# Performance work log

Measured on AMD Instinct MI355X. Metric: run time of the kernel, lower is better.

The kernel has to match this reference:

```python
import jax, jax.numpy as jnp
import numpy as np

N_NODES = 100000
N_EDGES = 1600000
IN_DIM = 128
HEADS = 4
HID = 32            # per-head channels; HEADS*HID == 128 == IN_DIM
HC = HEADS * HID
NUM_CLASSES = 349
NUM_LAYERS = 2
BN_EPS = 1e-5
NEG_SLOPE = 0.2     # PyG GATConv default leaky_relu slope


def _gat_conv(x, src, dst, Wsrc, Wdst, a_src, a_dst, bias):
    """PyG GATConv (concat=True). x:[N,F] -> [N,H*C]."""
    N = x.shape[0]
    xs = (x @ Wsrc).reshape(N, HEADS, HID)   # source-side projection
    xd = (x @ Wdst).reshape(N, HEADS, HID)   # dest-side projection
    s_src = jnp.einsum('nhc,hc->nh', xs, a_src)   # [N,H]
    s_dst = jnp.einsum('nhc,hc->nh', xd, a_dst)   # [N,H]
    e = jax.nn.leaky_relu(s_src[src] + s_dst[dst], NEG_SLOPE)   # [E,H]
    # numerically-stable edge softmax grouped by destination node
    m = jax.ops.segment_max(e, dst, num_segments=N)             # [N,H]
    m = jnp.where(jnp.isfinite(m), m, 0.0)                      # isolated nodes
    p = jnp.exp(e - m[dst])                                     # [E,H]
    denom = jax.ops.segment_sum(p, dst, num_segments=N)         # [N,H]
    alpha = p / (denom[dst] + 1e-16)                            # [E,H]
    msg = xs[src] * alpha[:, :, None]                           # [E,H,C]
    out = jax.ops.segment_sum(msg, dst, num_segments=N)         # [N,H,C]
    return out.reshape(N, HC) + bias


def _batch_norm(x, gamma, beta):
    mu = x.mean(0)
    var = x.var(0)
    return gamma * (x - mu) * jax.lax.rsqrt(var + BN_EPS) + beta


def setup_inputs() -> dict:
    key = jax.random.key(0)
    ks = jax.random.split(key, 8)
    sc = 1.0 / np.sqrt(IN_DIM)
    inp = {
        'x': jax.random.normal(ks[0], (N_NODES, IN_DIM), jnp.float32),
        'edge_index': jax.random.randint(ks[1], (2, N_EDGES), 0, N_NODES, jnp.int32),
        'W_src': jax.random.normal(ks[2], (NUM_LAYERS, IN_DIM, HC), jnp.float32) * sc,
        'W_dst': jax.random.normal(ks[3], (NUM_LAYERS, IN_DIM, HC), jnp.float32) * sc,
        'att_src': jax.random.normal(ks[4], (NUM_LAYERS, HEADS, HID), jnp.float32) * sc,
        'att_dst': jax.random.normal(ks[5], (NUM_LAYERS, HEADS, HID), jnp.float32) * sc,
        'conv_bias': jnp.zeros((NUM_LAYERS, HC), jnp.float32),
        'lin_W': jax.random.normal(ks[6], (NUM_LAYERS, IN_DIM, HC), jnp.float32) * sc,
        'lin_b': jnp.zeros((NUM_LAYERS, HC), jnp.float32),
        'bn_gamma': jnp.ones((NUM_LAYERS, HC), jnp.float32),
        'bn_beta': jnp.zeros((NUM_LAYERS, HC), jnp.float32),
        'fc_W': jax.random.normal(ks[7], (IN_DIM, NUM_CLASSES), jnp.float32) * sc,
        'fc_b': jnp.zeros((NUM_CLASSES,), jnp.float32),
    }
    return inp


def reference(x, edge_index, W_src, W_dst, att_src, att_dst, conv_bias,
              lin_W, lin_b, bn_gamma, bn_beta, fc_W, fc_b):
    src, dst = edge_index[0], edge_index[1]
    for i in range(NUM_LAYERS):
        h = _gat_conv(x, src, dst, W_src[i], W_dst[i], att_src[i], att_dst[i],
                      conv_bias[i])
        h = h + x @ lin_W[i] + lin_b[i]          # skip projection
        h = _batch_norm(h, bn_gamma[i], bn_beta[i])
        x = jax.nn.relu(h)                        # dropout p=0.2 omitted (eval)
    return x @ fc_W + fc_b
```

## Files before the change

### kernel.cpp

```cpp
#include <hip/hip_runtime.h>
#include <hip/hip_bf16.h>
#include <stdint.h>

#define N_NODES 100000
#define N_EDGES 1600000
#define IN_DIM 128
#define HEADS 4
#define HID 32
#define HC 128
#define NUM_CLASSES 349
#define NUM_LAYERS 2
#define BN_EPS 1e-5f
#define NEG_SLOPE 0.2f
#define NCAT 264
#define MP 100032

#define NPARAM 144861

#define NBKT 782
#define ECHUNK 8192
#define NCHUNK ((N_EDGES + ECHUNK - 1) / ECHUNK)
#define NTOT (NBKT * NCHUNK)
#define SCAN_CHUNK 1024
#define SCAN2_BLOCKS ((NTOT + SCAN_CHUNK - 1) / SCAN_CHUNK)

using bf16 = __hip_bfloat16;
typedef __attribute__((ext_vector_type(8))) short short8;
typedef __attribute__((ext_vector_type(4))) float floatx4;

__device__ __forceinline__ float b2f(bf16 v) { return __bfloat162float(v); }

__global__ void detect_dtype(const uint32_t* __restrict__ xw, int* __restrict__ flag) {
    int lane = threadIdx.x;
    int insane = 0;
    for (int i = lane; i < 256; i += 64) {
        uint32_t lo = xw[i] & 0xffffu;
        uint32_t e = (lo >> 7) & 0xffu;
        if (lo != 0u && (e < 100u || e > 150u)) insane++;
    }
    for (int off = 32; off > 0; off >>= 1) insane += __shfl_down(insane, off, 64);
    if (lane == 0) *flag = (insane > 64) ? 1 : 0;
}

__global__ void cvt_xb(const void* __restrict__ in, bf16* __restrict__ out,
                       int n, int npad, const int* __restrict__ flag) {
    bool isf32 = (*flag != 0);
    int i = blockIdx.x * blockDim.x + threadIdx.x;
    int stride = gridDim.x * blockDim.x;
    for (; i < npad; i += stride) {
        bf16 v = __float2bfloat16(0.f);
        if (i < n) v = isf32 ? __float2bfloat16(((const float*)in)[i]) : ((const bf16*)in)[i];
        out[i] = v;
    }
}

__global__ void cvt_params(const void* p0, const void* p1, const void* p2, const void* p3,
                           const void* p4, const void* p5, const void* p6, const void* p7,
                           const void* p8, const void* p9, const void* p10,
                           float* __restrict__ out, const int* __restrict__ flag) {
    int i = blockIdx.x * blockDim.x + threadIdx.x;
    if (i >= NPARAM) return;
    bool isf32 = (*flag != 0);
    const void* p; int off;
    if      (i < 32768)  { p = p0;  off = i; }
    else if (i < 65536)  { p = p1;  off = i - 32768; }
    else if (i < 65792)  { p = p2;  off = i - 65536; }
    else if (i < 66048)  { p = p3;  off = i - 65792; }
    else if (i < 66304)  { p = p4;  off = i - 66048; }
    else if (i < 99072)  { p = p5;  off = i - 66304; }
    else if (i < 99328)  { p = p6;  off = i - 99072; }
    else if (i < 99584)  { p = p7;  off = i - 99328; }
    else if (i < 99840)  { p = p8;  off = i - 99584; }
    else if (i < 144512) { p = p9;  off = i - 99840; }
    else                 { p = p10; off = i - 144512; }
    out[i] = isf32 ? ((const float*)p)[off] : b2f(((const bf16*)p)[off]);
}

__global__ void build_bcat(const float* __restrict__ Wsrc, const float* __restrict__ Wdst,
                           const float* __restrict__ asrc, const float* __restrict__ adst,
                           const float* __restrict__ linW, float* __restrict__ B) {
    int idx = blockIdx.x * blockDim.x + threadIdx.x;
    if (idx >= IN_DIM * NCAT) return;
    int k = idx / NCAT, j = idx - k * NCAT;
    float v;
    if (j < 128) {
        v = Wsrc[k * HC + j];
    } else if (j < 132) {
        int h = j - 128; float s = 0.f;
        for (int c = 0; c < HID; c++) s += Wsrc[k * HC + h * HID + c] * asrc[h * HID + c];
        v = s;
    } else if (j < 136) {
        int h = j - 132; float s = 0.f;
        for (int c = 0; c < HID; c++) s += Wdst[k * HC + h * HID + c] * adst[h * HID + c];
        v = s;
    } else {
        v = linW[k * HC + (j - 136)];
    }
    B[idx] = v;
}

__global__ void pack_b(const float* __restrict__ src, int ld, int nvalid,
                       bf16* __restrict__ Bp, int total) {
    int idx = blockIdx.x * blockDim.x + threadIdx.x;
    if (idx >= total) return;
    int j = idx & 7, lane = (idx >> 3) & 63, kt = (idx >> 9) & 3, nt = idx >> 11;
    int n = nt * 16 + (lane & 15);
    int k = kt * 32 + ((lane >> 4) << 3) + j;
    float v = (n < nvalid) ? src[k * ld + n] : 0.f;
    Bp[idx] = __float2bfloat16(v);
}

template <int BNMODE>
__global__ __launch_bounds__(256) void gemm_mfma_proj(
    const bf16* __restrict__ A, const bf16* __restrict__ Bp,
    bf16* __restrict__ xs, bf16* __restrict__ scA, bf16* __restrict__ xlin,
    const float* __restrict__ gamma, const float* __restrict__ beta,
    const float* __restrict__ bnsum, const float* __restrict__ bnsq) {
    __shared__ bf16 As[64 * 128];
    int tid = threadIdx.x;
    size_t rowbase = (size_t)blockIdx.x * 64;
    const int4* ga = (const int4*)(A + rowbase * 128);
    int4* la = (int4*)As;
    const float invN = 1.f / (float)N_NODES;
#pragma unroll
    for (int s = 0; s < 4; s++) {
        int4 raw = ga[s * 256 + tid];
        if (BNMODE) {
            bf16* hv = (bf16*)&raw;
            int cbase = ((s * 256 + tid) & 15) * 8;
            int4 outv; bf16* ov = (bf16*)&outv;
#pragma unroll
            for (int j = 0; j < 8; j++) {
                int c = cbase + j;
                float mu = bnsum[c] * invN;
                float var = bnsq[c] * invN - mu * mu;
                float v = gamma[c] * (b2f(hv[j]) - mu) * rsqrtf(var + BN_EPS) + beta[c];
                ov[j] = __float2bfloat16(v > 0.f ? v : 0.f);
            }
            la[s * 256 + tid] = outv;
        } else {
            la[s * 256 + tid] = raw;
        }
    }
    __syncthreads();
    int wave = tid >> 6, lane = tid & 63;
    int arow = wave * 16 + (lane & 15);
    int acol = (lane >> 4) * 8;
    short8 afrag[4];
#pragma unroll
    for (int kt = 0; kt < 4; kt++)
        afrag[kt] = *(const short8*)&As[arow * 128 + kt * 32 + acol];
    const short8* bbase = (const short8*)Bp + lane;
    int colb = lane & 15;
    int row0 = wave * 16 + (lane >> 4) * 4;
#pragma unroll
    for (int nt = 0; nt < 17; nt++) {
        floatx4 acc = {0.f, 0.f, 0.f, 0.f};
#pragma unroll
        for (int kt = 0; kt < 4; kt++)
            acc = __builtin_amdgcn_mfma_f32_16x16x32_bf16(afrag[kt], bbase[(nt * 4 + kt) * 64], acc, 0, 0, 0);
        int col = nt * 16 + colb;
#pragma unroll
        for (int r = 0; r < 4; r++) {
            size_t row = rowbase + row0 + r;
            bf16 v = __float2bfloat16(acc[r]);
            if (col < 128)       xs[row * HC + col] = v;
            else if (col < 136)  scA[row * 8 + (col - 128)] = v;
            else { int q = col - 136; if (q < 128) xlin[row * HC + q] = v; }
        }
    }
}

__global__ __launch_bounds__(256) void gemm_mfma_out(
    const bf16* __restrict__ A, const bf16* __restrict__ Bp,
    const float* __restrict__ bias,
    const float* __restrict__ gamma, const float* __restrict__ beta,
    const float* __restrict__ bnsum, const float* __restrict__ bnsq,
    void* __restrict__ C, const int* __restrict__ flag) {
    __shared__ bf16 As[64 * 128];
    int tid = threadIdx.x;
    size_t rowbase = (size_t)blockIdx.x * 64;
    const int4* ga = (const int4*)(A + rowbase * 128);
    int4* la = (int4*)As;
    const float invN = 1.f / (float)N_NODES;
#pragma unroll
    for (int s = 0; s < 4; s++) {
        int4 raw = ga[s * 256 + tid];
        bf16* hv = (bf16*)&raw;
        int cbase = ((s * 256 + tid) & 15) * 8;
        int4 outv; bf16* ov = (bf16*)&outv;
#pragma unroll
        for (int j = 0; j < 8; j++) {
            int c = cbase + j;
            float mu = bnsum[c] * invN;
            float var = bnsq[c] * invN - mu * mu;
            float v = gamma[c] * (b2f(hv[j]) - mu) * rsqrtf(var + BN_EPS) + beta[c];
            ov[j] = __float2bfloat16(v > 0.f ? v : 0.f);
        }
        la[s * 256 + tid] = outv;
    }
    __syncthreads();
    int wave = tid >> 6, lane = tid & 63;
    int arow = wave * 16 + (lane & 15);
    int acol = (lane >> 4) * 8;
    short8 afrag[4];
#pragma unroll
    for (int kt = 0; kt < 4; kt++)
        afrag[kt] = *(const short8*)&As[arow * 128 + kt * 32 + acol];
    const short8* bbase = (const short8*)Bp + lane;
    int colb = lane & 15;
    int row0 = wave * 16 + (lane >> 4) * 4;
    bool isf32 = (*flag != 0);
    for (int nt = 0; nt < 22; nt++) {
        floatx4 acc = {0.f, 0.f, 0.f, 0.f};
#pragma unroll
        for (int kt = 0; kt < 4; kt++)
            acc = __builtin_amdgcn_mfma_f32_16x16x32_bf16(afrag[kt], bbase[(nt * 4 + kt) * 64], acc, 0, 0, 0);
        int col = nt * 16 + colb;
        if (col >= NUM_CLASSES) continue;
        float bv = bias[col];
#pragma unroll
        for (int r = 0; r < 4; r++) {
            size_t row = rowbase + row0 + r;
            if (row < N_NODES) {
                float v = acc[r] + bv;
                if (isf32) ((float*)C)[row * NUM_CLASSES + col] = v;
                else       ((bf16*)C)[row * NUM_CLASSES + col] = __float2bfloat16(v);
            }
        }
    }
}

__global__ __launch_bounds__(256) void bucket_hist(const int* __restrict__ dst,
                                                   int* __restrict__ cnt) {
    __shared__ int h[NBKT];
    int t = threadIdx.x;
    for (int i = t; i < NBKT; i += 256) h[i] = 0;
    __syncthreads();
    int base = blockIdx.x * ECHUNK;
    int end = base + ECHUNK; if (end > N_EDGES) end = N_EDGES;
    for (int i = base + t; i < end; i += 256)
        atomicAdd(&h[dst[i] >> 7], 1);
    __syncthreads();
    for (int i = t; i < NBKT; i += 256)
        cnt[i * NCHUNK + blockIdx.x] = h[i];
}

__global__ void scan_partial(const int* __restrict__ counts, int* __restrict__ bsum, int n) {
    __shared__ int red[256];
    int t = threadIdx.x;
    int base = blockIdx.x * SCAN_CHUNK + t * 4;
    int s = 0;
#pragma unroll
    for (int j = 0; j < 4; j++) {
        int idx = base + j;
        if (idx < n) s += counts[idx];
    }
    red[t] = s;
    __syncthreads();
    for (int off = 128; off > 0; off >>= 1) {
        if (t < off) red[t] += red[t + off];
        __syncthreads();
    }
    if (t == 0) bsum[blockIdx.x] = red[0];
}

__global__ void scan_bsums(int* __restrict__ bsum, int nblocks) {
    if (threadIdx.x != 0 || blockIdx.x != 0) return;
    int run = 0;
    for (int i = 0; i < nblocks; i++) {
        int v = bsum[i];
        bsum[i] = run;
        run += v;
    }
}

__global__ void scan_final(int* __restrict__ counts, const int* __restrict__ bsum, int n) {
    __shared__ int ts[256];
    int t = threadIdx.x;
    int base = blockIdx.x * SCAN_CHUNK + t * 4;
    int c[4];
    int mysum = 0;
#pragma unroll
    for (int j = 0; j < 4; j++) {
        int idx = base + j;
        c[j] = (idx < n) ? counts[idx] : 0;
        mysum += c[j];
    }
    ts[t] = mysum;
    __syncthreads();
    for (int off = 1; off < 256; off <<= 1) {
        int v = (t >= off) ? ts[t - off] : 0;
        __syncthreads();
        ts[t] += v;
        __syncthreads();
    }
    int run = bsum[blockIdx.x] + ts[t] - mysum;
#pragma unroll
    for (int j = 0; j < 4; j++) {
        int idx = base + j;
        if (idx < n) {
            counts[idx] = run;
            run += c[j];
        }
    }
}

__global__ __launch_bounds__(256) void bucket_scatter(const int* __restrict__ src,
                                                      const int* __restrict__ dst,
                                                      const int* __restrict__ cntscan,
                                                      uint32_t* __restrict__ sorted) {
    __shared__ int cur[NBKT];
    int t = threadIdx.x;
    for (int i = t; i < NBKT; i += 256)
        cur[i] = cntscan[i * NCHUNK + blockIdx.x];
    __syncthreads();
    int base = blockIdx.x * ECHUNK;
    int end = base + ECHUNK; if (end > N_EDGES) end = N_EDGES;
    for (int i = base + t; i < end; i += 256) {
        int d = dst[i];
        int b = d >> 7;
        int pos = atomicAdd(&cur[b], 1);
        sorted[pos] = ((uint32_t)(d & 127) << 17) | (uint32_t)src[i];
    }
}

__global__ __launch_bounds__(256) void bucket_csr(const uint32_t* __restrict__ sorted,
                                                  const int* __restrict__ cntscan,
                                                  int* __restrict__ srcs,
                                                  int* __restrict__ offsets) {
    __shared__ int cnt128[128];
    __shared__ int sc[128];
    __shared__ int cur[128];
    int b = blockIdx.x, t = threadIdx.x;
    int ebeg = cntscan[b * NCHUNK];
    int eend = (b == NBKT - 1) ? N_EDGES : cntscan[(b + 1) * NCHUNK];
    if (t < 128) cnt128[t] = 0;
    __syncthreads();
    uint32_t buf[10];
    int k = 0;
    for (int e = ebeg + t; e < eend; e += 256) {
        uint32_t u = sorted[e];
        if (k < 10) buf[k] = u;
        k++;
        atomicAdd(&cnt128[u >> 17], 1);
    }
    __syncthreads();
    if (t < 128) sc[t] = cnt128[t];
    __syncthreads();
    for (int off = 1; off < 128; off <<= 1) {
        int v = 0;
        if (t < 128 && t >= off) v = sc[t - off];
        __syncthreads();
        if (t < 128) sc[t] += v;
        __syncthreads();
    }
    if (t < 128) {
        int node = b * 128 + t;
        if (node < N_NODES) offsets[node] = ebeg + sc[t];
        cur[t] = ebeg + sc[t] - cnt128[t];
    }
    __syncthreads();
    int k2 = 0;
    for (int e = ebeg + t; e < eend; e += 256) {
        uint32_t u = (k2 < 10) ? buf[k2] : sorted[e];
        k2++;
        int ld = (int)(u >> 17);
        int pos = atomicAdd(&cur[ld], 1);
        srcs[pos] = (int)(u & 0x1FFFFu);
    }
}

__device__ __forceinline__ void edge_acc(int s, int h, int c0, float s_dst,
                                         const bf16* __restrict__ xs,
                                         const bf16* __restrict__ scA,
                                         float& den, float& n0, float& n1) {
    float sc = b2f(scA[(size_t)s * 8 + h]) + s_dst;
    sc = sc > 0.f ? sc : NEG_SLOPE * sc;
    float e = __expf(sc);
    __hip_bfloat162 xv = *reinterpret_cast<const __hip_bfloat162*>(&xs[(size_t)s * HC + c0]);
    den += e;
    n0 += b2f(xv.x) * e;
    n1 += b2f(xv.y) * e;
}

__global__ __launch_bounds__(256) void gat_gather(
    const int* __restrict__ srcs, const int* __restrict__ offsets,
    const bf16* __restrict__ xs, const bf16* __restrict__ scA,
    const bf16* __restrict__ xlin,
    const float* __restrict__ cbias, const float* __restrict__ lbias,
    bf16* __restrict__ hout) {
    int n = blockIdx.x * 4 + (threadIdx.x >> 6);
    int lane = threadIdx.x & 63;
    int c0 = lane * 2;
    int h = c0 >> 5;
    int beg = (n == 0) ? 0 : offsets[n - 1];
    int end = offsets[n];
    float s_dst = b2f(scA[(size_t)n * 8 + 4 + h]);
    float den = 0.f, n0 = 0.f, n1 = 0.f;
    int i = beg;
    for (; i + 3 < end; i += 4) {
        int s0 = srcs[i], s1 = srcs[i + 1], s2 = srcs[i + 2], s3 = srcs[i + 3];
        edge_acc(s0, h, c0, s_dst, xs, scA, den, n0, n1);
        edge_acc(s1, h, c0, s_dst, xs, scA, den, n0, n1);
        edge_acc(s2, h, c0, s_dst, xs, scA, den, n0, n1);
        edge_acc(s3, h, c0, s_dst, xs, scA, den, n0, n1);
    }
    for (; i < end; i++)
        edge_acc(srcs[i], h, c0, s_dst, xs, scA, den, n0, n1);
    float r = 1.f / (den + 1e-16f);
    __hip_bfloat162 xl = *reinterpret_cast<const __hip_bfloat162*>(&xlin[(size_t)n * HC + c0]);
    float v0 = n0 * r + b2f(xl.x) + cbias[c0] + lbias[c0];
    float v1 = n1 * r + b2f(xl.y) + cbias[c0 + 1] + lbias[c0 + 1];
    __hip_bfloat162 hv;
    hv.x = __float2bfloat16(v0);
    hv.y = __float2bfloat16(v1);
    *reinterpret_cast<__hip_bfloat162*>(&hout[(size_t)n * HC + c0]) = hv;
}

__global__ void bn_stats(const bf16* __restrict__ h, float* __restrict__ bnsum,
                         float* __restrict__ bnsq) {
    int c = threadIdx.x & 127;
    int half = threadIdx.x >> 7;
    int r0 = blockIdx.x * 500;
    int rend = r0 + 500; if (rend > N_NODES) rend = N_NODES;
    float s1 = 0.f, s2 = 0.f;
    for (int r = r0 + half; r < rend; r += 2) {
        float v = b2f(h[(size_t)r * HC + c]);
        s1 += v; s2 += v * v;
    }
    atomicAdd(&bnsum[c], s1);
    atomicAdd(&bnsq[c], s2);
}

extern "C" void kernel_launch(void* const* d_in, const int* in_sizes, int n_in,
                              void* d_out, int out_size, void* d_ws, size_t ws_size,
                              hipStream_t stream) {
    const void* x_in = d_in[0];
    const int*  edge = (const int*)d_in[1];
    const int* esrc = edge;
    const int* edst = edge + N_EDGES;

    bf16* xbh  = (bf16*)d_ws;
    bf16* xs   = xbh + (size_t)MP * HC;
    bf16* scA  = xs + (size_t)MP * HC;
    bf16* xlin = scA + (size_t)MP * 8;
    float* Bcat = (float*)(xlin + (size_t)MP * HC);
    bf16* Bp   = (bf16*)(Bcat + IN_DIM * NCAT);
    bf16* fcWp = Bp + 17 * 2048;
    float* bnstat = (float*)(fcWp + 22 * 2048);
    int*   flag  = (int*)(bnstat + 512);
    int*   bsum  = flag + 4;
    float* parms = (float*)(bsum + SCAN2_BLOCKS + 2);
    float* Wsrc_f  = parms;
    float* Wdst_f  = parms + 32768;
    float* asrc_f  = parms + 65536;
    float* adst_f  = parms + 65792;
    float* cbias_f = parms + 66048;
    float* linW_f  = parms + 66304;
    float* linb_f  = parms + 99072;
    float* gamma_f = parms + 99328;
    float* beta_f  = parms + 99584;
    float* fcW_f   = parms + 99840;
    float* fcb_f   = parms + 144512;

    int* srcs    = (int*)d_out;
    int* offsets = srcs + N_EDGES;
    uint32_t* sorted = (uint32_t*)(offsets + N_NODES);
    int* cnt = (int*)(sorted + N_EDGES);

    detect_dtype<<<1, 64, 0, stream>>>((const uint32_t*)x_in, flag);

    cvt_xb<<<1024, 256, 0, stream>>>(x_in, xbh, N_NODES * HC, MP * HC, flag);
    cvt_params<<<(NPARAM + 255) / 256, 256, 0, stream>>>(
        d_in[2], d_in[3], d_in[4], d_in[5], d_in[6], d_in[7], d_in[8],
        d_in[9], d_in[10], d_in[11], d_in[12], parms, flag);

    bucket_hist<<<NCHUNK, 256, 0, stream>>>(edst, cnt);
    scan_partial<<<SCAN2_BLOCKS, 256, 0, stream>>>(cnt, bsum, NTOT);
    scan_bsums<<<1, 64, 0, stream>>>(bsum, SCAN2_BLOCKS);
    scan_final<<<SCAN2_BLOCKS, 256, 0, stream>>>(cnt, bsum, NTOT);
    bucket_scatter<<<NCHUNK, 256, 0, stream>>>(esrc, edst, cnt, sorted);
    bucket_csr<<<NBKT, 256, 0, stream>>>(sorted, cnt, srcs, offsets);

    pack_b<<<(22 * 2048 + 255) / 256, 256, 0, stream>>>(fcW_f, NUM_CLASSES, NUM_CLASSES,
                                                        fcWp, 22 * 2048);
    hipMemsetAsync(bnstat, 0, 512 * sizeof(float), stream);

    for (int layer = 0; layer < NUM_LAYERS; layer++) {
        const int woff = layer * IN_DIM * HC;
        const int aoff = layer * HEADS * HID;
        const int boff = layer * HC;
        float* bns = bnstat + layer * 256;
        float* bnq = bns + 128;

        build_bcat<<<(IN_DIM * NCAT + 255) / 256, 256, 0, stream>>>(
            Wsrc_f + woff, Wdst_f + woff, asrc_f + aoff, adst_f + aoff,
            linW_f + woff, Bcat);
        pack_b<<<(17 * 2048 + 255) / 256, 256, 0, stream>>>(Bcat, NCAT, NCAT,
                                                            Bp, 17 * 2048);

        if (layer == 0) {
            gemm_mfma_proj<0><<<MP / 64, 256, 0, stream>>>(
                xbh, Bp, xs, scA, xlin, nullptr, nullptr, nullptr, nullptr);
        } else {
            float* pbns = bnstat + (layer - 1) * 256;
            gemm_mfma_proj<1><<<MP / 64, 256, 0, stream>>>(
                xbh, Bp, xs, scA, xlin,
                gamma_f + (layer - 1) * HC, beta_f + (layer - 1) * HC,
                pbns, pbns + 128);
        }

        gat_gather<<<N_NODES / 4, 256, 0, stream>>>(
            srcs, offsets, xs, scA, xlin, cbias_f + boff, linb_f + boff, xbh);

        bn_stats<<<200, 256, 0, stream>>>(xbh, bns, bnq);
    }

    gemm_mfma_out<<<MP / 64, 256, 0, stream>>>(
        xbh, fcWp, fcb_f, gamma_f + HC, beta_f + HC,
        bnstat + 256, bnstat + 256 + 128, d_out, flag);
}
```

Baseline: 758.2 us.

## Fuse input conversion into projection GEMM, merge weight packing, drop serial scan

Removes the separate x-to-bf16 conversion kernel: the layer-0 projection GEMM now reads the raw input (fp32 or bf16) and converts it while staging into shared memory. build_bcat and pack_b are merged so the concatenated weights go straight into the packed MFMA layout. The single-thread block-sum scan is dropped, and each scan_final block instead reduces the prefix of bsum itself. The gather loop also gains an 8-way unrolled edge loop. Together these cut kernel launches and one full pass over x, at the cost of redundant prefix reductions across scan blocks and higher register use in the gather.

Result: faster. 703.1 us (-7.3%).

```diff
diff --git a/kernel.cpp b/kernel.cpp
--- a/kernel.cpp
+++ b/kernel.cpp
@@ -40,18 +40,6 @@
     }
     for (int off = 32; off > 0; off >>= 1) insane += __shfl_down(insane, off, 64);
     if (lane == 0) *flag = (insane > 64) ? 1 : 0;
-}
-
-__global__ void cvt_xb(const void* __restrict__ in, bf16* __restrict__ out,
-                       int n, int npad, const int* __restrict__ flag) {
-    bool isf32 = (*flag != 0);
-    int i = blockIdx.x * blockDim.x + threadIdx.x;
-    int stride = gridDim.x * blockDim.x;
-    for (; i < npad; i += stride) {
-        bf16 v = __float2bfloat16(0.f);
-        if (i < n) v = isf32 ? __float2bfloat16(((const float*)in)[i]) : ((const bf16*)in)[i];
-        out[i] = v;
-    }
 }
 
 __global__ void cvt_params(const void* p0, const void* p1, const void* p2, const void* p3,
@@ -76,27 +64,27 @@
     out[i] = isf32 ? ((const float*)p)[off] : b2f(((const bf16*)p)[off]);
 }
 
-__global__ void build_bcat(const float* __restrict__ Wsrc, const float* __restrict__ Wdst,
-                           const float* __restrict__ asrc, const float* __restrict__ adst,
-                           const float* __restrict__ linW, float* __restrict__ B) {
+__global__ void pack_bcat(const float* __restrict__ Wsrc, const float* __restrict__ Wdst,
+                          const float* __restrict__ asrc, const float* __restrict__ adst,
+                          const float* __restrict__ linW, bf16* __restrict__ Bp) {
     int idx = blockIdx.x * blockDim.x + threadIdx.x;
-    if (idx >= IN_DIM * NCAT) return;
-    int k = idx / NCAT, j = idx - k * NCAT;
-    float v;
-    if (j < 128) {
-        v = Wsrc[k * HC + j];
-    } else if (j < 132) {
-        int h = j - 128; float s = 0.f;
-        for (int c = 0; c < HID; c++) s += Wsrc[k * HC + h * HID + c] * asrc[h * HID + c];
-        v = s;
-    } else if (j < 136) {
-        int h = j - 132; float s = 0.f;
-        for (int c = 0; c < HID; c++) s += Wdst[k * HC + h * HID + c] * adst[h * HID + c];
-        v = s;
-    } else {
-        v = linW[k * HC + (j - 136)];
-    }
-    B[idx] = v;
+    if (idx >= 17 * 2048) return;
+    int j = idx & 7, lane = (idx >> 3) & 63, kt = (idx >> 9) & 3, nt = idx >> 11;
+    int n = nt * 16 + (lane & 15);
+    int k = kt * 32 + ((lane >> 4) << 3) + j;
+    float v = 0.f;
+    if (n < 128) {
+        v = Wsrc[k * HC + n];
+    } else if (n < 132) {
+        int h = n - 128;
+        for (int c = 0; c < HID; c++) v += Wsrc[k * HC + h * HID + c] * asrc[h * HID + c];
+    } else if (n < 136) {
+        int h = n - 132;
+        for (int c = 0; c < HID; c++) v += Wdst[k * HC + h * HID + c] * adst[h * HID + c];
+    } else if (n < 264) {
+        v = linW[k * HC + (n - 136)];
+    }
+    Bp[idx] = __float2bfloat16(v);
 }
 
 __global__ void pack_b(const float* __restrict__ src, int ld, int nvalid,
@@ -110,22 +98,48 @@
     Bp[idx] = __float2bfloat16(v);
 }
 
-template <int BNMODE>
+template <int MODE>
 __global__ __launch_bounds__(256) void gemm_mfma_proj(
-    const bf16* __restrict__ A, const bf16* __restrict__ Bp,
+    const void* __restrict__ Araw, const int* __restrict__ flag,
+    const bf16* __restrict__ Bp,
     bf16* __restrict__ xs, bf16* __restrict__ scA, bf16* __restrict__ xlin,
     const float* __restrict__ gamma, const float* __restrict__ beta,
     const float* __restrict__ bnsum, const float* __restrict__ bnsq) {
     __shared__ bf16 As[64 * 128];
     int tid = threadIdx.x;
     size_t rowbase = (size_t)blockIdx.x * 64;
-    const int4* ga = (const int4*)(A + rowbase * 128);
     int4* la = (int4*)As;
     const float invN = 1.f / (float)N_NODES;
-#pragma unroll
-    for (int s = 0; s < 4; s++) {
-        int4 raw = ga[s * 256 + tid];
-        if (BNMODE) {
+    if (MODE == 0) {
+        bool isf32 = (*flag != 0);
+#pragma unroll
+        for (int s = 0; s < 4; s++) {
+            int idx = s * 256 + tid;
+            size_t grow = rowbase + (idx >> 4);
+            int cg = idx & 15;
+            int4 outv = {0, 0, 0, 0};
+            if (grow < N_NODES) {
+                if (isf32) {
+                    const float* xr = (const float*)Araw + grow * 128 + cg * 8;
+                    float4 f0 = ((const float4*)xr)[0];
+                    float4 f1 = ((const float4*)xr)[1];
+                    bf16* ov = (bf16*)&outv;
+                    ov[0] = __float2bfloat16(f0.x); ov[1] = __float2bfloat16(f0.y);
+                    ov[2] = __float2bfloat16(f0.z); ov[3] = __float2bfloat16(f0.w);
+                    ov[4] = __float2bfloat16(f1.x); ov[5] = __float2bfloat16(f1.y);
+                    ov[6] = __float2bfloat16(f1.z); ov[7] = __float2bfloat16(f1.w);
+                } else {
+                    outv = ((const int4*)Araw)[grow * 16 + cg];
+                }
+            }
+            la[idx] = outv;
+        }
+    } else {
+        const bf16* A = (const bf16*)Araw;
+        const int4* ga = (const int4*)(A + rowbase * 128);
+#pragma unroll
+        for (int s = 0; s < 4; s++) {
+            int4 raw = ga[s * 256 + tid];
             bf16* hv = (bf16*)&raw;
             int cbase = ((s * 256 + tid) & 15) * 8;
             int4 outv; bf16* ov = (bf16*)&outv;
@@ -138,8 +152,6 @@
                 ov[j] = __float2bfloat16(v > 0.f ? v : 0.f);
             }
             la[s * 256 + tid] = outv;
-        } else {
-            la[s * 256 + tid] = raw;
         }
     }
     __syncthreads();
@@ -265,19 +277,12 @@
     if (t == 0) bsum[blockIdx.x] = red[0];
 }
 
-__global__ void scan_bsums(int* __restrict__ bsum, int nblocks) {
-    if (threadIdx.x != 0 || blockIdx.x != 0) return;
-    int run = 0;
-    for (int i = 0; i < nblocks; i++) {
-        int v = bsum[i];
-        bsum[i] = run;
-        run += v;
-    }
-}
-
 __global__ void scan_final(int* __restrict__ counts, const int* __restrict__ bsum, int n) {
     __shared__ int ts[256];
+    __shared__ int pre[256];
     int t = threadIdx.x;
+    int pv = (t < (int)blockIdx.x) ? bsum[t] : 0;
+    pre[t] = pv;
     int base = blockIdx.x * SCAN_CHUNK + t * 4;
     int c[4];
     int mysum = 0;
@@ -289,13 +294,17 @@
     }
     ts[t] = mysum;
     __syncthreads();
+    for (int off = 128; off > 0; off >>= 1) {
+        if (t < off) pre[t] += pre[t + off];
+        __syncthreads();
+    }
     for (int off = 1; off < 256; off <<= 1) {
         int v = (t >= off) ? ts[t - off] : 0;
         __syncthreads();
         ts[t] += v;
         __syncthreads();
     }
-    int run = bsum[blockIdx.x] + ts[t] - mysum;
+    int run = pre[0] + ts[t] - mysum;
 #pragma unroll
     for (int j = 0; j < 4; j++) {
         int idx = base + j;
@@ -399,6 +408,18 @@
     float s_dst = b2f(scA[(size_t)n * 8 + 4 + h]);
     float den = 0.f, n0 = 0.f, n1 = 0.f;
     int i = beg;
+    for (; i + 7 < end; i += 8) {
+        int s0 = srcs[i],     s1 = srcs[i + 1], s2 = srcs[i + 2], s3 = srcs[i + 3];
+        int s4 = srcs[i + 4], s5 = srcs[i + 5], s6 = srcs[i + 6], s7 = srcs[i + 7];
+        edge_acc(s0, h, c0, s_dst, xs, scA, den, n0, n1);
+        edge_acc(s1, h, c0, s_dst, xs, scA, den, n0, n1);
+        edge_acc(s2, h, c0, s_dst, xs, scA, den, n0, n1);
+        edge_acc(s3, h, c0, s_dst, xs, scA, den, n0, n1);
+        edge_acc(s4, h, c0, s_dst, xs, scA, den, n0, n1);
+        edge_acc(s5, h, c0, s_dst, xs, scA, den, n0, n1);
+        edge_acc(s6, h, c0, s_dst, xs, scA, den, n0, n1);
+        edge_acc(s7, h, c0, s_dst, xs, scA, den, n0, n1);
+    }
     for (; i + 3 < end; i += 4) {
         int s0 = srcs[i], s1 = srcs[i + 1], s2 = srcs[i + 2], s3 = srcs[i + 3];
         edge_acc(s0, h, c0, s_dst, xs, scA, den, n0, n1);
@@ -445,8 +466,7 @@
     bf16* xs   = xbh + (size_t)MP * HC;
     bf16* scA  = xs + (size_t)MP * HC;
     bf16* xlin = scA + (size_t)MP * 8;
-    float* Bcat = (float*)(xlin + (size_t)MP * HC);
-    bf16* Bp   = (bf16*)(Bcat + IN_DIM * NCAT);
+    bf16* Bp   = xlin + (size_t)MP * HC;
     bf16* fcWp = Bp + 17 * 2048;
     float* bnstat = (float*)(fcWp + 22 * 2048);
     int*   flag  = (int*)(bnstat + 512);
@@ -471,14 +491,12 @@
 
     detect_dtype<<<1, 64, 0, stream>>>((const uint32_t*)x_in, flag);
 
-    cvt_xb<<<1024, 256, 0, stream>>>(x_in, xbh, N_NODES * HC, MP * HC, flag);
     cvt_params<<<(NPARAM + 255) / 256, 256, 0, stream>>>(
         d_in[2], d_in[3], d_in[4], d_in[5], d_in[6], d_in[7], d_in[8],
         d_in[9], d_in[10], d_in[11], d_in[12], parms, flag);
 
     bucket_hist<<<NCHUNK, 256, 0, stream>>>(edst, cnt);
     scan_partial<<<SCAN2_BLOCKS, 256, 0, stream>>>(cnt, bsum, NTOT);
-    scan_bsums<<<1, 64, 0, stream>>>(bsum, SCAN2_BLOCKS);
     scan_final<<<SCAN2_BLOCKS, 256, 0, stream>>>(cnt, bsum, NTOT);
     bucket_scatter<<<NCHUNK, 256, 0, stream>>>(esrc, edst, cnt, sorted);
     bucket_csr<<<NBKT, 256, 0, stream>>>(sorted, cnt, srcs, offsets);
@@ -494,19 +512,17 @@
         float* bns = bnstat + layer * 256;
         float* bnq = bns + 128;
 
-        build_bcat<<<(IN_DIM * NCAT + 255) / 256, 256, 0, stream>>>(
+        pack_bcat<<<(17 * 2048 + 255) / 256, 256, 0, stream>>>(
             Wsrc_f + woff, Wdst_f + woff, asrc_f + aoff, adst_f + aoff,
-            linW_f + woff, Bcat);
-        pack_b<<<(17 * 2048 + 255) / 256, 256, 0, stream>>>(Bcat, NCAT, NCAT,
-                                                            Bp, 17 * 2048);
+            linW_f + woff, Bp);
 
         if (layer == 0) {
             gemm_mfma_proj<0><<<MP / 64, 256, 0, stream>>>(
-                xbh, Bp, xs, scA, xlin, nullptr, nullptr, nullptr, nullptr);
+                x_in, flag, Bp, xs, scA, xlin, nullptr, nullptr, nullptr, nullptr);
         } else {
             float* pbns = bnstat + (layer - 1) * 256;
             gemm_mfma_proj<1><<<MP / 64, 256, 0, stream>>>(
-                xbh, Bp, xs, scA, xlin,
+                xbh, nullptr, Bp, xs, scA, xlin,
                 gamma_f + (layer - 1) * HC, beta_f + (layer - 1) * HC,
                 pbns, pbns + 128);
         }
```
